# Kernel optimization log

Hardware: AMD Instinct MI355X
Metric: run time of the kernel (lower is better)

The kernel has to match this reference:

```python
import jax, jax.numpy as jnp
import numpy as np
from jax import lax

B, TX, TY = 32, 512, 1024
D, H, FN, KS, L = 256, 2, 1024, 9, 4
WORD_NUM = 256
NEG = -1e9


def sinusoid_table(seq_len, d):
    pos = np.arange(seq_len)[:, None].astype(np.float64)
    i = np.arange(d)[None, :]
    angle = pos / np.power(10000.0, 2 * (i // 2) / d)
    table = np.zeros((seq_len, d))
    table[:, 0::2] = np.sin(angle[:, 0::2])
    table[:, 1::2] = np.cos(angle[:, 1::2])
    return jnp.asarray(table, dtype=jnp.float32)


def setup_inputs():
    key = jax.random.key(0)
    ks = jax.random.split(key, 16)
    s = 0.02
    w = lambda k, shape: jax.random.normal(k, shape, jnp.float32) * s
    embed = w(ks[4], (WORD_NUM, D)).at[0].set(0.0)  # padding_idx=0
    return dict(
        tokens=jax.random.randint(ks[0], (B, TX), 1, WORD_NUM),
        src_lengths=jax.random.randint(ks[1], (B,), TX // 2, TX + 1),
        mel_lengths=jax.random.randint(ks[2], (B,), TY // 2, TY + 1),
        value=jax.random.normal(ks[3], (B, TX, TY), jnp.float32),
        embed=embed,
        pos_enc=sinusoid_table(TX, D),
        wq=w(ks[5], (L, D, D)), bq=jnp.zeros((L, D), jnp.float32),
        wk=w(ks[6], (L, D, D)), bk=jnp.zeros((L, D), jnp.float32),
        wv=w(ks[7], (L, D, D)), bv=jnp.zeros((L, D), jnp.float32),
        wo=w(ks[8], (L, D, D)), bo=jnp.zeros((L, D), jnp.float32),
        ln1_g=jnp.ones((L, D), jnp.float32), ln1_b=jnp.zeros((L, D), jnp.float32),
        c1_w=w(ks[9], (L, FN, D, KS)), c1_b=jnp.zeros((L, FN), jnp.float32),
        c2_w=w(ks[10], (L, D, FN, KS)), c2_b=jnp.zeros((L, D), jnp.float32),
        ln2_g=jnp.ones((L, D), jnp.float32), ln2_b=jnp.zeros((L, D), jnp.float32),
    )


def layer_norm(x, g, b, eps=1e-5):
    m = jnp.mean(x, axis=-1, keepdims=True)
    v = jnp.mean(jnp.square(x - m), axis=-1, keepdims=True)
    return (x - m) * lax.rsqrt(v + eps) * g + b


def conv1d(x, w, b):
    # x: [B, C_in, T], w: [C_out, C_in, K]
    p = (w.shape[-1] - 1) // 2
    y = lax.conv_general_dilated(x, w, (1,), [(p, p)],
                                 dimension_numbers=('NCH', 'OIH', 'NCH'))
    return y + b[None, :, None]


def maximum_path(value, mask):
    # Monotonic alignment search DP. value, mask: [B, Tx, Ty]
    b, tx, ty = value.shape
    value = value * mask
    x_range = jnp.arange(tx)[None, :]

    def fwd_step(v, inp):
        j, val_j = inp
        v0 = jnp.concatenate([jnp.full((b, 1), NEG, value.dtype), v[:, :-1]], axis=1)
        max_mask = v >= v0
        v_max = jnp.where(max_mask, v, v0)
        v_new = jnp.where(x_range <= j, v_max + val_j, NEG)
        return v_new, max_mask

    _, directions = lax.scan(fwd_step, jnp.zeros((b, tx), value.dtype),
                             (jnp.arange(ty), jnp.moveaxis(value, 2, 0)))
    directions = jnp.where(jnp.moveaxis(mask, 2, 0).astype(bool), directions, True)

    idx0 = mask[:, :, 0].sum(1).astype(jnp.int32) - 1  # last valid x index per batch
    brange = jnp.arange(b)

    def bwd_step(idx, dir_j):
        col = jax.nn.one_hot(idx, tx, dtype=value.dtype)
        idx_new = idx + dir_j[brange, idx].astype(jnp.int32) - 1
        return idx_new, col

    _, cols = lax.scan(bwd_step, idx0, directions, reverse=True)
    path = jnp.moveaxis(cols, 0, 2) * mask  # [B, Tx, Ty]
    return path


def reference(tokens, src_lengths, mel_lengths, value, embed, pos_enc,
              wq, bq, wk, bk, wv, bv, wo, bo, ln1_g, ln1_b,
              c1_w, c1_b, c2_w, c2_b, ln2_g, ln2_b):
    bsz, tx = tokens.shape
    pad = jnp.arange(tx)[None, :] >= src_lengths[:, None]      # [B,Tx] True=pad
    mel_pad = jnp.arange(TY)[None, :] >= mel_lengths[:, None]  # [B,Ty]
    dk = D // H
    scale = 1.0 / np.sqrt(dk).astype(np.float32)

    x = embed[tokens] + pos_enc[None, :tx, :]
    for l in range(L):
        # --- multi-head self-attention ---
        res = x
        q = (x @ wq[l] + bq[l]).reshape(bsz, tx, H, dk)
        k = (x @ wk[l] + bk[l]).reshape(bsz, tx, H, dk)
        v = (x @ wv[l] + bv[l]).reshape(bsz, tx, H, dk)
        attn = jnp.einsum('bqhd,bkhd->bhqk', q, k) * scale
        attn = jnp.where(pad[:, None, None, :], NEG, attn)
        attn = jax.nn.softmax(attn, axis=-1)
        out = jnp.einsum('bhqk,bkhd->bqhd', attn, v).reshape(bsz, tx, D)
        x = layer_norm(out @ wo[l] + bo[l] + res, ln1_g[l], ln1_b[l])
        x = jnp.where(pad[:, :, None], 0.0, x)
        # --- conv1d FFN ---
        res = x
        h = x.transpose(0, 2, 1)
        h = jax.nn.relu(conv1d(h, c1_w[l], c1_b[l]))
        h = conv1d(h, c2_w[l], c2_b[l]).transpose(0, 2, 1)
        x = layer_norm(h + res, ln2_g[l], ln2_b[l])
        x = jnp.where(pad[:, :, None], 0.0, x)

    mas_mask = ((~pad)[:, :, None] & (~mel_pad)[:, None, :]).astype(jnp.float32)
    path = maximum_path(value, mas_mask)                 # [B,Tx,Ty]
    expanded = jnp.einsum('bxy,bxd->byd', path, x)       # [B,Ty,D]
    return expanded
```

## Files before the change

### kernel.cpp

```cpp
#include <hip/hip_runtime.h>

#define B_  32
#define TX  512
#define TY  1024
#define D_  256
#define H_  2
#define DK  128
#define FN  1024
#define NL  4
#define TXP 520
#define NEGF (-1e9f)

typedef __attribute__((ext_vector_type(4))) float f32x4;
typedef __attribute__((ext_vector_type(8))) short short8;
typedef __attribute__((ext_vector_type(4))) unsigned short ushort4v;

typedef __attribute__((address_space(3))) unsigned int lds_u32;
typedef __attribute__((address_space(1))) const unsigned int glb_u32;

__device__ __forceinline__ unsigned short f2bf(float x) {
  unsigned int u = __builtin_bit_cast(unsigned int, x);
  u += 0x7fffu + ((u >> 16) & 1u);
  return (unsigned short)(u >> 16);
}
__device__ __forceinline__ float bf2f(unsigned short x) {
  unsigned int u = ((unsigned int)x) << 16;
  return __builtin_bit_cast(float, u);
}
__device__ __forceinline__ void store_bf16x4(unsigned short* p, f32x4 v) {
  ushort4v o; o[0]=f2bf(v[0]); o[1]=f2bf(v[1]); o[2]=f2bf(v[2]); o[3]=f2bf(v[3]);
  *(ushort4v*)p = o;
}
__device__ __forceinline__ float wsum(float v) {
#pragma unroll
  for (int i = 1; i < 64; i <<= 1) v += __shfl_xor(v, i, 64);
  return v;
}
__device__ __forceinline__ float wmax(float v) {
#pragma unroll
  for (int i = 1; i < 64; i <<= 1) v = fmaxf(v, __shfl_xor(v, i, 64));
  return v;
}
__device__ __forceinline__ void gl_lds16(const unsigned short* g, unsigned short* l) {
  __builtin_amdgcn_global_load_lds((glb_u32*)g, (lds_u32*)l, 16, 0, 0);
}
__device__ __forceinline__ void gl_lds16f(const float* g, float* l) {
  __builtin_amdgcn_global_load_lds((glb_u32*)g, (lds_u32*)l, 16, 0, 0);
}
__device__ __forceinline__ float lane_shr1(float x) {
  int r = __builtin_amdgcn_update_dpp(0, __builtin_bit_cast(int, x), 0x138, 0xF, 0xF, false);
  return __builtin_bit_cast(float, r);
}

static const size_t OFF_XB   = 0;
static const size_t SZ_XB    = (size_t)B_*TXP*D_*2;
static const size_t OFF_HB   = OFF_XB + SZ_XB;
static const size_t SZ_HB    = (size_t)B_*TXP*FN*2;
static const size_t OFF_QKV  = OFF_HB + SZ_HB;
static const size_t SZ_QKV   = (size_t)B_*TX*768*2;
static const size_t OFF_S    = OFF_QKV + SZ_QKV;
static const size_t SZ_S     = (size_t)B_*H_*TX*TX*2;
static const size_t OFF_AO   = OFF_S + SZ_S;
static const size_t SZ_AO    = (size_t)B_*TX*D_*2;
static const size_t OFF_T1   = OFF_AO + SZ_AO;
static const size_t SZ_T1    = (size_t)B_*TX*D_*4;
static const size_t OFF_WQKV = OFF_T1 + SZ_T1;
static const size_t SZ_WQKV  = (size_t)NL*768*256*2;
static const size_t OFF_BQKV = OFF_WQKV + SZ_WQKV;
static const size_t SZ_BQKV  = (size_t)NL*768*4;
static const size_t OFF_WO   = OFF_BQKV + SZ_BQKV;
static const size_t SZ_WO    = (size_t)NL*256*256*2;
static const size_t OFF_WT1  = OFF_WO + SZ_WO;
static const size_t SZ_WT1   = (size_t)NL*9*1024*256*2;
static const size_t OFF_WT2  = OFF_WT1 + SZ_WT1;
static const size_t SZ_WT2   = SZ_WT1;
static const size_t OFF_DIRS = OFF_WT2 + SZ_WT2;
static const size_t SZ_DIRS  = (size_t)B_*TY*64;
static const size_t OFF_IDX  = OFF_DIRS + SZ_DIRS;

__global__ void repack_qkvw(const float* __restrict__ wq, const float* __restrict__ wk,
                            const float* __restrict__ wv, unsigned short* __restrict__ out) {
  int i = blockIdx.x*256 + threadIdx.x;
  if (i >= NL*768*256) return;
  int c = i & 255, j = (i >> 8) % 768, l = i / (768*256);
  const float* src = (j < 256) ? wq : (j < 512) ? wk : wv;
  out[i] = f2bf(src[((size_t)l*256 + c)*256 + (j & 255)]);
}
__global__ void repack_bias(const float* __restrict__ bq, const float* __restrict__ bk,
                            const float* __restrict__ bv, float* __restrict__ out) {
  int i = blockIdx.x*256 + threadIdx.x;
  if (i >= NL*768) return;
  int j = i % 768, l = i / 768;
  const float* src = (j < 256) ? bq : (j < 512) ? bk : bv;
  out[i] = src[l*256 + (j & 255)];
}
__global__ void repack_wo(const float* __restrict__ wo, unsigned short* __restrict__ out) {
  int i = blockIdx.x*256 + threadIdx.x;
  if (i >= NL*256*256) return;
  int c = i & 255, j = (i >> 8) & 255, l = i >> 16;
  out[i] = f2bf(wo[((size_t)l*256 + c)*256 + j]);
}
__global__ void repack_c1(const float* __restrict__ w, unsigned short* __restrict__ out) {
  int i = blockIdx.x*256 + threadIdx.x;
  if (i >= NL*9*1024*256) return;
  int c = i & 255; int rest = i >> 8;
  int f = rest & 1023; int rest2 = rest >> 10;
  int k = rest2 % 9, l = rest2 / 9;
  out[i] = f2bf(w[(((size_t)l*1024 + f)*256 + c)*9 + k]);
}
__global__ void repack_c2(const float* __restrict__ w, unsigned short* __restrict__ out) {
  int i = blockIdx.x*256 + threadIdx.x;
  if (i >= NL*9*256*1024) return;
  int f = i & 1023; int rest = i >> 10;
  int d = rest & 255; int rest2 = rest >> 8;
  int k = rest2 % 9, l = rest2 / 9;
  out[i] = f2bf(w[(((size_t)l*256 + d)*1024 + f)*9 + k]);
}
__global__ void zero_halo(unsigned short* __restrict__ xb, unsigned short* __restrict__ hb) {
  int i = blockIdx.x*256 + threadIdx.x;
  if (i < 65536) {
    int b = i >> 11, r = (i >> 8) & 7, c = i & 255;
    int row = (r < 4) ? r : (512 + r);
    xb[((size_t)b*TXP + row)*256 + c] = 0;
  } else {
    int j = i - 65536;
    if (j < 262144) {
      int b = j >> 13, r = (j >> 10) & 7, c = j & 1023;
      int row = (r < 4) ? r : (512 + r);
      hb[((size_t)b*TXP + row)*1024 + c] = 0;
    }
  }
}

__global__ __launch_bounds__(256) void embed_kernel(const int* __restrict__ tok,
    const float* __restrict__ emb, const float* __restrict__ pos,
    unsigned short* __restrict__ xbo ) {
  int row = blockIdx.x*4 + (threadIdx.x >> 6);
  int t = row & 511, b = row >> 9;
  int lane = threadIdx.x & 63;
  int tk = tok[row];
  f32x4 e = *(const f32x4*)(emb + (size_t)tk*256 + lane*4);
  f32x4 p = *(const f32x4*)(pos + (size_t)t*256 + lane*4);
  f32x4 v;
#pragma unroll
  for (int i = 0; i < 4; i++) v[i] = e[i] + p[i];
  store_bf16x4(xbo + ((size_t)b*TXP + t)*256 + lane*4, v);
}

__global__ __launch_bounds__(256) void gemm_mfma(
    const unsigned short* __restrict__ A, long long AbO, long long AhO, int Astr,
    const unsigned short* __restrict__ W, long long WbO, long long WhO, int Wstr,
    const float* __restrict__ bias,
    float* __restrict__ O32, long long O32bO, int O32str,
    unsigned short* __restrict__ O16, long long O16bO, long long O16hO, int O16str,
    int Cin, int Cout, int ks, int relu, int H,
    const int* __restrict__ sl, float scale, int maskmode,
    const int* __restrict__ tskip, int tmargin) {
  __shared__ unsigned short As[128*32];
  __shared__ unsigned short Ws[128*32];
  const int tid = threadIdx.x;
  int b, h;
  if (H == 2) { b = blockIdx.z >> 1; h = blockIdx.z & 1; }
  else        { b = blockIdx.z;      h = 0; }
  const int t0 = blockIdx.x * 128;
  const int f0 = blockIdx.y * 128;
  if (tskip && t0 >= tskip[b] + tmargin) return;
  const int slb = maskmode ? sl[b] : 0;
  const unsigned short* Ab = A + (size_t)b * AbO + (size_t)h * AhO;
  const unsigned short* Wb = W + (size_t)b * WbO + (size_t)h * WhO;
  const int lane = tid & 63, w = tid >> 6;
  const int wt = (w & 1) << 6, wf = (w >> 1) << 6;
  const int lr = lane & 15, lh = lane >> 4;
  const int r0 = tid >> 2, cg = (tid & 3) << 3;
  f32x4 zed = {0.f, 0.f, 0.f, 0.f};
  f32x4 acc[4][4];
#pragma unroll
  for (int i = 0; i < 4; i++)
#pragma unroll
    for (int j = 0; j < 4; j++) acc[i][j] = zed;

  const bool skipK = maskmode && (f0 >= slb);
  if (!skipK) {
    for (int k = 0; k < ks; ++k) {
      const unsigned short* AkB = Ab + (size_t)(t0 + k) * Astr;
      const unsigned short* WkB = Wb + ((size_t)k * Cout + f0) * Wstr;
      for (int c0 = 0; c0 < Cin; c0 += 32) {
        __syncthreads();
        gl_lds16(AkB + (size_t)r0 * Astr + (c0 + cg),        As + (size_t)tid * 8);
        gl_lds16(AkB + (size_t)(r0 + 64) * Astr + (c0 + cg), As + (size_t)(tid + 256) * 8);
        gl_lds16(WkB + (size_t)r0 * Wstr + (c0 + cg),        Ws + (size_t)tid * 8);
        gl_lds16(WkB + (size_t)(r0 + 64) * Wstr + (c0 + cg), Ws + (size_t)(tid + 256) * 8);
        __syncthreads();
        short8 af[4], bfv[4];
#pragma unroll
        for (int mt = 0; mt < 4; mt++) af[mt]  = *(const short8*)&As[(wt + mt*16 + lr)*32 + lh*8];
#pragma unroll
        for (int nt = 0; nt < 4; nt++) bfv[nt] = *(const short8*)&Ws[(wf + nt*16 + lr)*32 + lh*8];
#pragma unroll
        for (int mt = 0; mt < 4; mt++)
#pragma unroll
          for (int nt = 0; nt < 4; nt++)
            acc[mt][nt] = __builtin_amdgcn_mfma_f32_16x16x32_bf16(af[mt], bfv[nt], acc[mt][nt], 0, 0, 0);
      }
    }
  }
#pragma unroll
  for (int mt = 0; mt < 4; mt++) {
    int trow = t0 + wt + mt*16 + lh*4;
#pragma unroll
    for (int nt = 0; nt < 4; nt++) {
      int f = f0 + wf + nt*16 + lr;
      float bb = (!maskmode && bias) ? bias[f] : 0.f;
#pragma unroll
      for (int r = 0; r < 4; r++) {
        float v;
        if (maskmode) {
          v = acc[mt][nt][r] * scale;
          if (f >= slb) v = NEGF;
        } else {
          v = acc[mt][nt][r] + bb;
          if (relu) v = fmaxf(v, 0.f);
        }
        if (O32) O32[(size_t)b*O32bO + (size_t)(trow + r)*O32str + f] = v;
        if (O16) O16[(size_t)b*O16bO + (size_t)h*O16hO + (size_t)(trow + r)*O16str + f] = f2bf(v);
      }
    }
  }
}

__global__ __launch_bounds__(256) void vtrans_kernel(const unsigned short* __restrict__ qkv,
    const int* __restrict__ sl, unsigned short* __restrict__ VT) {
  const int z = blockIdx.z, b = z >> 1, h = z & 1;
  const int t0 = blockIdx.x << 5, d0 = blockIdx.y << 5;
  __shared__ unsigned short tile[32][33];
  const int tx = threadIdx.x, ty = threadIdx.y;
  const int slb = sl[b];
  const unsigned short* src = qkv + (size_t)b*TX*768 + 512 + h*DK;
#pragma unroll
  for (int i = 0; i < 4; i++)
    tile[ty + i*8][tx] = src[(size_t)(t0 + ty + i*8)*768 + d0 + tx];
  __syncthreads();
#pragma unroll
  for (int i = 0; i < 4; i++) {
    unsigned short v = (t0 + tx < slb) ? tile[tx][ty + i*8] : (unsigned short)0;
    VT[((size_t)z*DK + d0 + ty + i*8)*512 + t0 + tx] = v;
  }
}

__global__ __launch_bounds__(256) void softmax_kernel(unsigned short* __restrict__ S) {
  const int row = blockIdx.x*4 + (threadIdx.x >> 6);
  const int lane = threadIdx.x & 63;
  unsigned short* p = S + (size_t)row*512 + lane*8;
  short8 raw = *(const short8*)p;
  float a[8];
#pragma unroll
  for (int i = 0; i < 8; i++) a[i] = bf2f((unsigned short)raw[i]);
  float m = a[0];
#pragma unroll
  for (int i = 1; i < 8; i++) m = fmaxf(m, a[i]);
  m = wmax(m);
  float s = 0.f;
#pragma unroll
  for (int i = 0; i < 8; i++) { a[i] = __expf(a[i]-m); s += a[i]; }
  s = wsum(s);
  float inv = 1.f / s;
  short8 o;
#pragma unroll
  for (int i = 0; i < 8; i++) o[i] = (short)f2bf(a[i] * inv);
  *(short8*)p = o;
}

__global__ __launch_bounds__(256) void ln_kernel(const float* __restrict__ tin,
    const float* __restrict__ g, const float* __restrict__ bt, const int* __restrict__ sl,
    unsigned short* __restrict__ xbo ) {
  const int row = blockIdx.x*4 + (threadIdx.x >> 6);
  const int b = row >> 9, t = row & 511;
  const int lane = threadIdx.x & 63;
  unsigned short* xp = xbo + ((size_t)b*TXP + t)*256 + lane*4;
  f32x4 tv = *(const f32x4*)(tin + (size_t)row*256 + lane*4);
  ushort4v rv4 = *(const ushort4v*)xp;
  f32x4 s; float su = 0.f, sq = 0.f;
#pragma unroll
  for (int i = 0; i < 4; i++) {
    s[i] = tv[i] + bf2f(rv4[i]);
    su += s[i]; sq += s[i]*s[i];
  }
  su = wsum(su); sq = wsum(sq);
  float mean = su * (1.f/256.f);
  float var = fmaxf(sq * (1.f/256.f) - mean*mean, 0.f);
  float rs = rsqrtf(var + 1e-5f);
  f32x4 gg = *(const f32x4*)(g + lane*4);
  f32x4 bb = *(const f32x4*)(bt + lane*4);
  bool padr = (t >= sl[b]);
  f32x4 y;
#pragma unroll
  for (int i = 0; i < 4; i++) {
    float yy = (s[i]-mean)*rs*gg[i] + bb[i];
    y[i] = padr ? 0.f : yy;
  }
  store_bf16x4(xp, y);
}

__global__ __launch_bounds__(256) void transpose_mask(const float* __restrict__ value,
    const int* __restrict__ sl, const int* __restrict__ ml, float* __restrict__ vT) {
  const int b = blockIdx.z;
  const int x0 = blockIdx.y << 5, y0 = blockIdx.x << 5;
  __shared__ float tile[32][33];
  const int tx = threadIdx.x, ty = threadIdx.y;
  const int slb = sl[b], mlb = ml[b];
#pragma unroll
  for (int i = 0; i < 4; i++) {
    int x = x0 + ty + i*8, y = y0 + tx;
    float v = value[((size_t)b*TX + x)*TY + y];
    tile[ty + i*8][tx] = (x < slb && y < mlb) ? v : 0.f;
  }
  __syncthreads();
#pragma unroll
  for (int i = 0; i < 4; i++) {
    int y = y0 + ty + i*8, x = x0 + tx;
    vT[((size_t)b*TY + y)*TX + x] = tile[tx][ty + i*8];
  }
}

template<bool RAMP>
__device__ __forceinline__ void dp_comp8(
    int jb, const float* valbuf, unsigned long long* dll,
    float v[8], int lane, int xbase, unsigned int vmask, unsigned int fmask,
    bool lane0) {
  unsigned int w0 = 0, w1 = 0;
#pragma unroll
  for (int u = 0; u < 8; ++u) {
    const int j = jb*8 + u;
    f32x4 a0 = *(const f32x4*)(valbuf + u*512 + lane*8);
    f32x4 a1 = *(const f32x4*)(valbuf + u*512 + lane*8 + 4);
    float vp = lane_shr1(v[7]);
    if (lane0) vp = NEGF;
    unsigned int ge = 0;
#pragma unroll
    for (int i = 7; i >= 1; --i) {
      unsigned int g = (v[i] >= v[i-1]) ? 1u : 0u;
      ge = (ge << 1) | g;
      float nv = fmaxf(v[i], v[i-1]) + ((i < 4) ? a0[i] : a1[i-4]);
      if (RAMP) v[i] = (xbase + i <= j) ? nv : NEGF;
      else      v[i] = nv;
    }
    {
      unsigned int g = (v[0] >= vp) ? 1u : 0u;
      ge = (ge << 1) | g;
      float nv = fmaxf(v[0], vp) + a0[0];
      if (RAMP) v[0] = (xbase <= j) ? nv : NEGF;
      else      v[0] = nv;
    }
    unsigned int byt = (ge & vmask) | fmask;
    if (u < 4) w0 |= byt << (8*u); else w1 |= byt << (8*(u-4));
  }
  dll[jb*64 + lane] = ((unsigned long long)w1 << 32) | w0;
}

__global__ __launch_bounds__(64, 1) void dp_fused(const float* __restrict__ vT,
    const int* __restrict__ sl, const int* __restrict__ ml,
    int* __restrict__ idxout) {
  __shared__ float sval[3*4096];
  __shared__ unsigned long long dll[TY*8];
  unsigned char* dld = (unsigned char*)dll;
  const int b = blockIdx.x, lane = threadIdx.x;
  const int slb = sl[b], mlb = ml[b];
  const float* vb = vT + (size_t)b*TY*TX;
  const int xbase = lane*8;
  const bool lane0 = (lane == 0);
  unsigned int vmaskv = 0;
#pragma unroll
  for (int i = 0; i < 8; ++i) if (xbase + i < slb) vmaskv |= (1u << i);
  const unsigned int fmaskv = (~vmaskv) & 0xffu;
  float v[8];
#pragma unroll
  for (int i = 0; i < 8; ++i) v[i] = 0.f;
  const int jbEnd = (mlb + 7) >> 3;

  auto stage = [&](int jb, float* buf) {
    const float* src = vb + (size_t)jb*8*TX;
#pragma unroll
    for (int u = 0; u < 8; ++u) {
      gl_lds16f(src + u*TX + lane*4,       buf + u*512);
      gl_lds16f(src + u*TX + 256 + lane*4, buf + u*512 + 256);
    }
  };
  stage(0, sval);
  stage(1, sval + 4096);
  stage(2, sval + 8192);
  int buf = 0;
  int jb = 0;
  for (; jb < 64; ++jb) {
    if (jb + 2 < jbEnd)      asm volatile("s_waitcnt vmcnt(32)" ::: "memory");
    else if (jb + 1 < jbEnd) asm volatile("s_waitcnt vmcnt(16)" ::: "memory");
    else                     asm volatile("s_waitcnt vmcnt(0)"  ::: "memory");
    float* vbuf = sval + buf*4096;
    dp_comp8<true>(jb, vbuf, dll, v, lane, xbase, vmaskv, fmaskv, lane0);
    __builtin_amdgcn_sched_barrier(0);
    if (jb + 3 < jbEnd) stage(jb + 3, vbuf);
    buf = (buf == 2) ? 0 : buf + 1;
  }
  for (; jb < jbEnd; ++jb) {
    if (jb + 2 < jbEnd)      asm volatile("s_waitcnt vmcnt(32)" ::: "memory");
    else if (jb + 1 < jbEnd) asm volatile("s_waitcnt vmcnt(16)" ::: "memory");
    else                     asm volatile("s_waitcnt vmcnt(0)"  ::: "memory");
    float* vbuf = sval + buf*4096;
    dp_comp8<false>(jb, vbuf, dll, v, lane, xbase, vmaskv, fmaskv, lane0);
    __builtin_amdgcn_sched_barrier(0);
    if (jb + 3 < jbEnd) stage(jb + 3, vbuf);
    buf = (buf == 2) ? 0 : buf + 1;
  }
  for (int jj = mlb + lane; jj < TY; jj += 64) idxout[b*TY + jj] = -1;
  if (lane0) {
    int* ob = idxout + b*TY;
    int idx = slb - 1;
    int j = mlb - 1;
    while (j >= 6) {
      int o0 = idx >> 3;
      int o1 = (o0 > 0) ? (o0 - 1) : 0;
      unsigned int bc[7], ba[7];
#pragma unroll
      for (int s = 0; s < 7; ++s) {
        int r = j - s;
        int rbase = ((r >> 3) << 9) + (r & 7);
        bc[s] = dld[rbase + o0*8];
        ba[s] = dld[rbase + o1*8];
      }
#pragma unroll
      for (int s = 0; s < 7; ++s) {
        ob[j - s] = idx;
        unsigned int byt = ((idx >> 3) == o0) ? bc[s] : ba[s];
        idx += (int)((byt >> (idx & 7)) & 1u) - 1;
      }
      j -= 7;
    }
    while (j >= 0) {
      ob[j] = idx;
      unsigned int byt = dld[((j >> 3) << 9) + (j & 7) + (idx >> 3)*8];
      idx += (int)((byt >> (idx & 7)) & 1u) - 1;
      --j;
    }
  }
}

__global__ __launch_bounds__(256) void gather_kernel(const unsigned short* __restrict__ xbo,
    const int* __restrict__ idxout, float* __restrict__ out) {
  const int row = blockIdx.x*4 + (threadIdx.x >> 6);
  const int lane = threadIdx.x & 63;
  const int b = row >> 10;
  const int idx = idxout[row];
  f32x4 v;
  if (idx >= 0) {
    ushort4v r = *(const ushort4v*)(xbo + ((size_t)b*TXP + idx)*256 + lane*4);
#pragma unroll
    for (int i = 0; i < 4; i++) v[i] = bf2f(r[i]);
  } else { v[0]=0.f; v[1]=0.f; v[2]=0.f; v[3]=0.f; }
  *(f32x4*)(out + (size_t)row*256 + lane*4) = v;
}

extern "C" void kernel_launch(void* const* d_in, const int* in_sizes, int n_in,
                              void* d_out, int out_size, void* d_ws, size_t ws_size,
                              hipStream_t stream) {
  const int*   tokens = (const int*)d_in[0];
  const int*   sl     = (const int*)d_in[1];
  const int*   ml     = (const int*)d_in[2];
  const float* value  = (const float*)d_in[3];
  const float* emb    = (const float*)d_in[4];
  const float* pos    = (const float*)d_in[5];
  const float* wq     = (const float*)d_in[6];
  const float* bq     = (const float*)d_in[7];
  const float* wk     = (const float*)d_in[8];
  const float* bk     = (const float*)d_in[9];
  const float* wv     = (const float*)d_in[10];
  const float* bv     = (const float*)d_in[11];
  const float* wo     = (const float*)d_in[12];
  const float* bo     = (const float*)d_in[13];
  const float* ln1g   = (const float*)d_in[14];
  const float* ln1bb  = (const float*)d_in[15];
  const float* c1w    = (const float*)d_in[16];
  const float* c1b    = (const float*)d_in[17];
  const float* c2w    = (const float*)d_in[18];
  const float* c2b    = (const float*)d_in[19];
  const float* ln2g   = (const float*)d_in[20];
  const float* ln2bb  = (const float*)d_in[21];

  char* w8 = (char*)d_ws;
  unsigned short* xb     = (unsigned short*)(w8 + OFF_XB);
  unsigned short* hb     = (unsigned short*)(w8 + OFF_HB);
  unsigned short* qkvb   = (unsigned short*)(w8 + OFF_QKV);
  unsigned short* S      = (unsigned short*)(w8 + OFF_S);
  float*          vT     = (float*)(w8 + OFF_HB);
  unsigned short* VT     = (unsigned short*)(w8 + OFF_T1);
  unsigned short* ao     = (unsigned short*)(w8 + OFF_AO);
  float*          T1     = (float*)(w8 + OFF_T1);
  unsigned short* wqkv_r = (unsigned short*)(w8 + OFF_WQKV);
  float*          bqkv   = (float*)(w8 + OFF_BQKV);
  unsigned short* wo_r   = (unsigned short*)(w8 + OFF_WO);
  unsigned short* wt1r   = (unsigned short*)(w8 + OFF_WT1);
  unsigned short* wt2r   = (unsigned short*)(w8 + OFF_WT2);
  int*            idxout = (int*)(w8 + OFF_IDX);
  float*          out    = (float*)d_out;

  const float scale = 0.08838834764831843f;

  repack_qkvw<<<(NL*768*256 + 255)/256, 256, 0, stream>>>(wq, wk, wv, wqkv_r);
  repack_bias<<<(NL*768 + 255)/256, 256, 0, stream>>>(bq, bk, bv, bqkv);
  repack_wo<<<(NL*256*256 + 255)/256, 256, 0, stream>>>(wo, wo_r);
  repack_c1<<<(NL*9*1024*256 + 255)/256, 256, 0, stream>>>(c1w, wt1r);
  repack_c2<<<(NL*9*256*1024 + 255)/256, 256, 0, stream>>>(c2w, wt2r);

  transpose_mask<<<dim3(32, 16, 32), dim3(32, 8), 0, stream>>>(value, sl, ml, vT);
  dp_fused<<<32, 64, 0, stream>>>(vT, sl, ml, idxout);

  hipMemsetAsync(qkvb, 0, SZ_QKV, stream);

  zero_halo<<<(327680 + 255)/256, 256, 0, stream>>>(xb, hb);
  embed_kernel<<<4096, 256, 0, stream>>>(tokens, emb, pos, xb + 4*256);

  for (int l = 0; l < NL; l++) {
    gemm_mfma<<<dim3(4, 6, 32), 256, 0, stream>>>(
        xb + 4*256, (long long)TXP*256, 0, 256,
        wqkv_r + (size_t)l*768*256, 0, 0, 256,
        bqkv + l*768,
        nullptr, 0, 0,
        qkvb, (long long)TX*768, 0, 768,
        256, 768, 1, 0, 1, nullptr, 0.f, 0, sl, 0);
    gemm_mfma<<<dim3(4, 4, 64), 256, 0, stream>>>(
        qkvb, (long long)TX*768, 128, 768,
        qkvb + 256, (long long)TX*768, 128, 768,
        nullptr,
        nullptr, 0, 0,
        S, (long long)2*512*512, (long long)512*512, 512,
        128, 512, 1, 0, 2, sl, scale, 1, sl, 0);
    softmax_kernel<<<8192, 256, 0, stream>>>(S);
    vtrans_kernel<<<dim3(16, 4, 64), dim3(32, 8), 0, stream>>>(qkvb, sl, VT);
    gemm_mfma<<<dim3(4, 1, 64), 256, 0, stream>>>(
        S, (long long)2*512*512, (long long)512*512, 512,
        VT, (long long)2*DK*512, (long long)DK*512, 512,
        nullptr,
        nullptr, 0, 0,
        ao, (long long)TX*256, 128, 256,
        512, 128, 1, 0, 2, nullptr, 0.f, 0, sl, 0);
    gemm_mfma<<<dim3(4, 2, 32), 256, 0, stream>>>(
        ao, (long long)TX*256, 0, 256,
        wo_r + (size_t)l*256*256, 0, 0, 256,
        bo + l*256,
        T1, (long long)TX*256, 256,
        nullptr, 0, 0, 0,
        256, 256, 1, 0, 1, nullptr, 0.f, 0, sl, 0);
    ln_kernel<<<4096, 256, 0, stream>>>(T1, ln1g + l*256, ln1bb + l*256, sl, xb + 4*256);
    gemm_mfma<<<dim3(4, 8, 32), 256, 0, stream>>>(
        xb, (long long)TXP*256, 0, 256,
        wt1r + (size_t)l*9*1024*256, 0, 0, 256,
        c1b + l*1024,
        nullptr, 0, 0,
        hb + 4*1024, (long long)TXP*1024, 0, 1024,
        256, 1024, 9, 1, 1, nullptr, 0.f, 0, sl, 4);
    gemm_mfma<<<dim3(4, 2, 32), 256, 0, stream>>>(
        hb, (long long)TXP*1024, 0, 1024,
        wt2r + (size_t)l*9*256*1024, 0, 0, 1024,
        c2b + l*256,
        T1, (long long)TX*256, 256,
        nullptr, 0, 0, 0,
        1024, 256, 9, 0, 1, nullptr, 0.f, 0, sl, 0);
    ln_kernel<<<4096, 256, 0, stream>>>(T1, ln2g + l*256, ln2bb + l*256, sl, xb + 4*256);
  }

  gather_kernel<<<8192, 256, 0, stream>>>(xb + 4*256, idxout, out);
  (void)in_sizes; (void)n_in; (void)out_size; (void)ws_size;
}
```

Measured before the change: 2.200 ms.

## Template GEMM on kernel size with double-buffered LDS, XOR swizzle and conv A-tile reuse

```diff
diff --git a/kernel.cpp b/kernel.cpp
--- a/kernel.cpp
+++ b/kernel.cpp
@@ -147,17 +147,20 @@
   store_bf16x4(xbo + ((size_t)b*TXP + t)*256 + lane*4, v);
 }
 
+template<int KS>
 __global__ __launch_bounds__(256) void gemm_mfma(
     const unsigned short* __restrict__ A, long long AbO, long long AhO, int Astr,
     const unsigned short* __restrict__ W, long long WbO, long long WhO, int Wstr,
     const float* __restrict__ bias,
     float* __restrict__ O32, long long O32bO, int O32str,
     unsigned short* __restrict__ O16, long long O16bO, long long O16hO, int O16str,
-    int Cin, int Cout, int ks, int relu, int H,
+    int Cin, int Cout, int relu, int H,
     const int* __restrict__ sl, float scale, int maskmode,
     const int* __restrict__ tskip, int tmargin) {
-  __shared__ unsigned short As[128*32];
-  __shared__ unsigned short Ws[128*32];
+  constexpr int ASZ = (KS == 9) ? 6144 : 8192;
+  constexpr int WSZ = 8192;
+  __shared__ unsigned short As[ASZ];
+  __shared__ unsigned short Ws[WSZ];
   const int tid = threadIdx.x;
   int b, h;
   if (H == 2) { b = blockIdx.z >> 1; h = blockIdx.z & 1; }
@@ -171,7 +174,7 @@
   const int lane = tid & 63, w = tid >> 6;
   const int wt = (w & 1) << 6, wf = (w >> 1) << 6;
   const int lr = lane & 15, lh = lane >> 4;
-  const int r0 = tid >> 2, cg = (tid & 3) << 3;
+  const int r0 = tid >> 2, cq = tid & 3;
   f32x4 zed = {0.f, 0.f, 0.f, 0.f};
   f32x4 acc[4][4];
 #pragma unroll
@@ -179,28 +182,91 @@
 #pragma unroll
     for (int j = 0; j < 4; j++) acc[i][j] = zed;
 
+  auto rdfrag = [&](const unsigned short* base, int row) -> short8 {
+    return *(const short8*)&base[row*32 + (((lh ^ (row >> 1)) & 3) << 3)];
+  };
+
   const bool skipK = maskmode && (f0 >= slb);
   if (!skipK) {
-    for (int k = 0; k < ks; ++k) {
-      const unsigned short* AkB = Ab + (size_t)(t0 + k) * Astr;
-      const unsigned short* WkB = Wb + ((size_t)k * Cout + f0) * Wstr;
-      for (int c0 = 0; c0 < Cin; c0 += 32) {
-        __syncthreads();
-        gl_lds16(AkB + (size_t)r0 * Astr + (c0 + cg),        As + (size_t)tid * 8);
-        gl_lds16(AkB + (size_t)(r0 + 64) * Astr + (c0 + cg), As + (size_t)(tid + 256) * 8);
-        gl_lds16(WkB + (size_t)r0 * Wstr + (c0 + cg),        Ws + (size_t)tid * 8);
-        gl_lds16(WkB + (size_t)(r0 + 64) * Wstr + (c0 + cg), Ws + (size_t)(tid + 256) * 8);
-        __syncthreads();
+    const unsigned short* Arow = Ab + (size_t)t0 * Astr;
+    if constexpr (KS == 1) {
+      const int nC = Cin >> 5;
+      const unsigned short* Wrow = Wb + (size_t)f0 * Wstr;
+      auto st1 = [&](int c, int buf) {
+        const int cc = c << 5;
+#pragma unroll
+        for (int j = 0; j < 2; ++j) {
+          const int rl = j*64 + r0;
+          const int cs = ((cq ^ (rl >> 1)) & 3) << 3;
+          gl_lds16(Arow + (size_t)rl*Astr + cc + cs, As + buf*4096 + j*2048 + (size_t)tid*8);
+          gl_lds16(Wrow + (size_t)rl*Wstr + cc + cs, Ws + buf*4096 + j*2048 + (size_t)tid*8);
+        }
+      };
+      st1(0, 0);
+      for (int c = 0; c < nC; ++c) {
+        asm volatile("s_waitcnt vmcnt(0)" ::: "memory");
+        __builtin_amdgcn_s_barrier();
+        asm volatile("" ::: "memory");
+        if (c + 1 < nC) st1(c + 1, (c + 1) & 1);
+        const unsigned short* Ask = As + (c & 1)*4096;
+        const unsigned short* Wsk = Ws + (c & 1)*4096;
         short8 af[4], bfv[4];
 #pragma unroll
-        for (int mt = 0; mt < 4; mt++) af[mt]  = *(const short8*)&As[(wt + mt*16 + lr)*32 + lh*8];
-#pragma unroll
-        for (int nt = 0; nt < 4; nt++) bfv[nt] = *(const short8*)&Ws[(wf + nt*16 + lr)*32 + lh*8];
+        for (int mt = 0; mt < 4; mt++) af[mt]  = rdfrag(Ask, wt + mt*16 + lr);
+#pragma unroll
+        for (int nt = 0; nt < 4; nt++) bfv[nt] = rdfrag(Wsk, wf + nt*16 + lr);
 #pragma unroll
         for (int mt = 0; mt < 4; mt++)
 #pragma unroll
           for (int nt = 0; nt < 4; nt++)
             acc[mt][nt] = __builtin_amdgcn_mfma_f32_16x16x32_bf16(af[mt], bfv[nt], acc[mt][nt], 0, 0, 0);
+      }
+    } else {
+      auto stA9 = [&](int c0) {
+#pragma unroll
+        for (int j = 0; j < 3; ++j) {
+          const int rl = j*64 + r0;
+          const int cs = ((cq ^ (rl >> 1)) & 3) << 3;
+          gl_lds16(Arow + (size_t)rl*Astr + c0 + cs, As + j*2048 + (size_t)tid*8);
+        }
+      };
+      auto stW9 = [&](int c0, int k, int buf) {
+        const unsigned short* Wk = Wb + ((size_t)k * Cout + f0) * Wstr + c0;
+#pragma unroll
+        for (int j = 0; j < 2; ++j) {
+          const int rl = j*64 + r0;
+          const int cs = ((cq ^ (rl >> 1)) & 3) << 3;
+          gl_lds16(Wk + (size_t)rl*Wstr + cs, Ws + buf*4096 + j*2048 + (size_t)tid*8);
+        }
+      };
+      stA9(0); stW9(0, 0, 0);
+      for (int c0 = 0; c0 < Cin; c0 += 32) {
+        const bool last = (c0 + 32 >= Cin);
+#pragma unroll
+        for (int k = 0; k < 9; ++k) {
+          asm volatile("s_waitcnt vmcnt(0)" ::: "memory");
+          __builtin_amdgcn_s_barrier();
+          asm volatile("" ::: "memory");
+          if (k < 8) stW9(c0, k + 1, (k + 1) & 1);
+          const unsigned short* Wsk = Ws + (k & 1)*4096;
+          short8 af[4], bfv[4];
+#pragma unroll
+          for (int mt = 0; mt < 4; mt++) af[mt]  = rdfrag(As, k + wt + mt*16 + lr);
+#pragma unroll
+          for (int nt = 0; nt < 4; nt++) bfv[nt] = rdfrag(Wsk, wf + nt*16 + lr);
+          if (k == 8 && !last) {
+            asm volatile("s_waitcnt lgkmcnt(0)" ::: "memory");
+            __builtin_amdgcn_s_barrier();
+            asm volatile("" ::: "memory");
+            stA9(c0 + 32);
+            stW9(c0 + 32, 0, 0);
+          }
+#pragma unroll
+          for (int mt = 0; mt < 4; mt++)
+#pragma unroll
+            for (int nt = 0; nt < 4; nt++)
+              acc[mt][nt] = __builtin_amdgcn_mfma_f32_16x16x32_bf16(af[mt], bfv[nt], acc[mt][nt], 0, 0, 0);
+        }
       }
     }
   }
@@ -518,51 +584,51 @@
   embed_kernel<<<4096, 256, 0, stream>>>(tokens, emb, pos, xb + 4*256);
 
   for (int l = 0; l < NL; l++) {
-    gemm_mfma<<<dim3(4, 6, 32), 256, 0, stream>>>(
+    gemm_mfma<1><<<dim3(4, 6, 32), 256, 0, stream>>>(
         xb + 4*256, (long long)TXP*256, 0, 256,
         wqkv_r + (size_t)l*768*256, 0, 0, 256,
         bqkv + l*768,
         nullptr, 0, 0,
         qkvb, (long long)TX*768, 0, 768,
-        256, 768, 1, 0, 1, nullptr, 0.f, 0, sl, 0);
-    gemm_mfma<<<dim3(4, 4, 64), 256, 0, stream>>>(
+        256, 768, 0, 1, nullptr, 0.f, 0, sl, 0);
+    gemm_mfma<1><<<dim3(4, 4, 64), 256, 0, stream>>>(
         qkvb, (long long)TX*768, 128, 768,
         qkvb + 256, (long long)TX*768, 128, 768,
         nullptr,
         nullptr, 0, 0,
         S, (long long)2*512*512, (long long)512*512, 512,
-        128, 512, 1, 0, 2, sl, scale, 1, sl, 0);
+        128, 512, 0, 2, sl, scale, 1, sl, 0);
     softmax_kernel<<<8192, 256, 0, stream>>>(S);
     vtrans_kernel<<<dim3(16, 4, 64), dim3(32, 8), 0, stream>>>(qkvb, sl, VT);
-    gemm_mfma<<<dim3(4, 1, 64), 256, 0, stream>>>(
+    gemm_mfma<1><<<dim3(4, 1, 64), 256, 0, stream>>>(
         S, (long long)2*512*512, (long long)512*512, 512,
         VT, (long long)2*DK*512, (long long)DK*512, 512,
         nullptr,
         nullptr, 0, 0,
         ao, (long long)TX*256, 128, 256,
-        512, 128, 1, 0, 2, nullptr, 0.f, 0, sl, 0);
-    gemm_mfma<<<dim3(4, 2, 32), 256, 0, stream>>>(
+        512, 128, 0, 2, nullptr, 0.f, 0, sl, 0);
+    gemm_mfma<1><<<dim3(4, 2, 32), 256, 0, stream>>>(
         ao, (long long)TX*256, 0, 256,
         wo_r + (size_t)l*256*256, 0, 0, 256,
         bo + l*256,
         T1, (long long)TX*256, 256,
         nullptr, 0, 0, 0,
-        256, 256, 1, 0, 1, nullptr, 0.f, 0, sl, 0);
+        256, 256, 0, 1, nullptr, 0.f, 0, sl, 0);
     ln_kernel<<<4096, 256, 0, stream>>>(T1, ln1g + l*256, ln1bb + l*256, sl, xb + 4*256);
-    gemm_mfma<<<dim3(4, 8, 32), 256, 0, stream>>>(
+    gemm_mfma<9><<<dim3(4, 8, 32), 256, 0, stream>>>(
         xb, (long long)TXP*256, 0, 256,
         wt1r + (size_t)l*9*1024*256, 0, 0, 256,
         c1b + l*1024,
         nullptr, 0, 0,
         hb + 4*1024, (long long)TXP*1024, 0, 1024,
-        256, 1024, 9, 1, 1, nullptr, 0.f, 0, sl, 4);
-    gemm_mfma<<<dim3(4, 2, 32), 256, 0, stream>>>(
+        256, 1024, 1, 1, nullptr, 0.f, 0, sl, 4);
+    gemm_mfma<9><<<dim3(4, 2, 32), 256, 0, stream>>>(
         hb, (long long)TXP*1024, 0, 1024,
         wt2r + (size_t)l*9*256*1024, 0, 0, 1024,
         c2b + l*256,
         T1, (long long)TX*256, 256,
         nullptr, 0, 0, 0,
-        1024, 256, 9, 0, 1, nullptr, 0.f, 0, sl, 0);
+        1024, 256, 0, 1, nullptr, 0.f, 0, sl, 0);
     ln_kernel<<<4096, 256, 0, stream>>>(T1, ln2g + l*256, ln2bb + l*256, sl, xb + 4*256);
   }
 
```

Result: faster. 2.028 ms (-7.8%).
